# Kernel tuning notes

Hardware: AMD Instinct MI355X
Metric: run time of the kernel (lower is better)

Reference implementation:

```python
import jax, jax.numpy as jnp
import numpy as np

D = 2048
H = 16
HD = D // H
B = 2
T = 2048
EPS = 1e-6


def setup_inputs() -> dict:
    key = jax.random.key(0)
    ks = jax.random.split(key, 12)
    s = lambda fan_in: 1.0 / np.sqrt(fan_in)
    inp = {
        "x": jax.random.normal(ks[0], (B, T, D), dtype=jnp.float32),
        "mask": jnp.tril(jnp.ones((T, T), dtype=jnp.int32))[None, None],  # [1,1,T,T] causal
        "w_norm1": jnp.ones((D,), dtype=jnp.float32),
        "w_qkv": jax.random.normal(ks[1], (D, 3 * D), dtype=jnp.float32) * s(D),
        "b_qkv": jnp.zeros((3 * D,), dtype=jnp.float32),
        "w_proj": jax.random.normal(ks[2], (D, D), dtype=jnp.float32) * s(D),
        "b_proj": jnp.zeros((D,), dtype=jnp.float32),
        "w_norm2": jnp.ones((D,), dtype=jnp.float32),
        "w_fc1": jax.random.normal(ks[3], (D, 4 * D), dtype=jnp.float32) * s(D),
        "b_fc1": jnp.zeros((4 * D,), dtype=jnp.float32),
        "w_fc2": jax.random.normal(ks[4], (4 * D, D), dtype=jnp.float32) * s(4 * D),
        "b_fc2": jnpp_zeros((D,)) if False else jnp.zeros((D,), dtype=jnp.float32),
    }
    return inp


def _rmsnorm(x, w):
    # n = ||x||_2 / sqrt(d); out = x / (n + eps) * w  (matches source exactly)
    n = jnp.sqrt(jnp.sum(x * x, axis=-1, keepdims=True)) * (x.shape[-1] ** -0.5)
    return x / (n + EPS) * w


def _rope(q, k):
    # q,k: [B,H,T,HD]; half-split (non-interleaved) RoPE
    half = HD // 2
    idx = jnp.arange(half, dtype=jnp.float32)
    pos = jnp.arange(T, dtype=jnp.float32)[:, None]
    rates = jnp.power(10000.0, -2.0 * idx / HD)
    theta = pos * rates  # [T, half]
    cos, sin = jnp.cos(theta), jnp.sin(theta)

    def apply(x):
        x1, x2 = x[..., :half], x[..., half:]
        return jnp.concatenate([x1 * cos - x2 * sin, x1 * sin + x2 * cos], axis=-1)

    return apply(q), apply(k)


def reference(x, mask, w_norm1, w_qkv, b_qkv, w_proj, b_proj,
              w_norm2, w_fc1, b_fc1, w_fc2, b_fc2):
    # --- attention branch ---
    h = _rmsnorm(x, w_norm1)
    qkv = h @ w_qkv + b_qkv  # [B,T,3D]
    q, k, v = jnp.split(qkv, 3, axis=-1)
    q = q.reshape(B, T, H, HD).transpose(0, 2, 1, 3)
    k = k.reshape(B, T, H, HD).transpose(0, 2, 1, 3)
    v = v.reshape(B, T, H, HD).transpose(0, 2, 1, 3)
    q, k = _rope(q, k)
    att = jnp.einsum("bhqd,bhkd->bhqk", q, k) * (HD ** -0.5)
    att = jnp.where(mask == 0, -jnp.inf, att)
    att = jax.nn.softmax(att, axis=-1)
    y = jnp.einsum("bhqk,bhkd->bhqd", att, v)
    y = y.transpose(0, 2, 1, 3).reshape(B, T, D)
    x = x + (y @ w_proj + b_proj)
    # --- MLP branch ---
    h2 = _rmsnorm(x, w_norm2)
    h2 = jax.nn.silu(h2 @ w_fc1 + b_fc1)
    x = x + (h2 @ w_fc2 + b_fc2)
    return x
```

## Files before the change

### kernel.cpp

```cpp
#include <hip/hip_runtime.h>
#include <math.h>

typedef unsigned short u16;
typedef unsigned int u32;
typedef __attribute__((ext_vector_type(8))) short short8v;
typedef __attribute__((ext_vector_type(4))) float float4v;

#define T_SEQ 2048
#define D_MODEL 2048
#define N_HEADS 16
#define EPSV 1e-6f
#define MROWS 4096
#define MB (1024ull * 1024ull)

__device__ __forceinline__ u16 f2bf(float f) {
  union { float f; u32 u; } v; v.f = f;
  u32 r = v.u + 0x7fffu + ((v.u >> 16) & 1u);
  return (u16)(r >> 16);
}
__device__ __forceinline__ float bf2f(u16 h) {
  union { u32 u; float f; } v; v.u = ((u32)h) << 16;
  return v.f;
}
__device__ __forceinline__ void gl16(const void* g, void* l) {
  __builtin_amdgcn_global_load_lds(
      (const __attribute__((address_space(1))) void*)g,
      (__attribute__((address_space(3))) void*)l, 16, 0, 0);
}

__global__ __launch_bounds__(256) void rmsnorm_split_kernel(
    const float* __restrict__ x, const float* __restrict__ w,
    u16* __restrict__ oh, u16* __restrict__ ol) {
  const int row = blockIdx.x;
  const float* xr = x + (size_t)row * D_MODEL;

  float ss = 0.f;
#pragma unroll
  for (int it = 0; it < 2; ++it) {
    int i = threadIdx.x + it * 256;
    float4 v = ((const float4*)xr)[i];
    ss += v.x * v.x + v.y * v.y + v.z * v.z + v.w * v.w;
  }
#pragma unroll
  for (int off = 32; off >= 1; off >>= 1) ss += __shfl_xor(ss, off, 64);
  __shared__ float red[4];
  if ((threadIdx.x & 63) == 0) red[threadIdx.x >> 6] = ss;
  __syncthreads();
  const float tot = red[0] + red[1] + red[2] + red[3];
  const float n = sqrtf(tot) * 0.022097086912079608f;
  const float inv = 1.0f / (n + EPSV);

  u16* ohr = oh + (size_t)row * D_MODEL;
  u16* olr = ol + (size_t)row * D_MODEL;
#pragma unroll
  for (int it = 0; it < 2; ++it) {
    int i = threadIdx.x + it * 256;
    float4 v = ((const float4*)xr)[i];
    float4 wv = ((const float4*)w)[i];
    float o[4] = {v.x * inv * wv.x, v.y * inv * wv.y, v.z * inv * wv.z,
                  v.w * inv * wv.w};
    ushort4 h4, l4;
    h4.x = f2bf(o[0]); l4.x = f2bf(o[0] - bf2f(h4.x));
    h4.y = f2bf(o[1]); l4.y = f2bf(o[1] - bf2f(h4.y));
    h4.z = f2bf(o[2]); l4.z = f2bf(o[2] - bf2f(h4.z));
    h4.w = f2bf(o[3]); l4.w = f2bf(o[3] - bf2f(h4.w));
    ((ushort4*)ohr)[i] = h4;
    ((ushort4*)olr)[i] = l4;
  }
}

__global__ __launch_bounds__(256) void splitT_kernel(
    const float* __restrict__ W, u16* __restrict__ Th, u16* __restrict__ Tl,
    int K, int N) {
  __shared__ float tile[32][33];
  const int tx = threadIdx.x, ty = threadIdx.y;
  const int n0 = blockIdx.x * 32, k0 = blockIdx.y * 32;
#pragma unroll
  for (int i = 0; i < 4; ++i)
    tile[ty + i * 8][tx] = W[(size_t)(k0 + ty + i * 8) * N + n0 + tx];
  __syncthreads();
#pragma unroll
  for (int i = 0; i < 4; ++i) {
    const float v = tile[tx][ty + i * 8];
    const int n = n0 + ty + i * 8, k = k0 + tx;
    const u16 h = f2bf(v);
    Th[(size_t)n * K + k] = h;
    Tl[(size_t)n * K + k] = f2bf(v - bf2f(h));
  }
}

template <int OUT>
__global__ __launch_bounds__(256) void mgemm_kernel(
    const u16* __restrict__ Ah, const u16* __restrict__ Al,
    const u16* __restrict__ Bh, const u16* __restrict__ Bl,
    const float* __restrict__ bias, const float* __restrict__ res,
    float* __restrict__ C, u16* __restrict__ Ch, u16* __restrict__ Cl,
    int N, int K) {
  __shared__ __align__(16) u16 LAH[2][4096];
  __shared__ __align__(16) u16 LAL[2][4096];
  __shared__ __align__(16) u16 LBH[2][4096];
  __shared__ __align__(16) u16 LBL[2][4096];

  const int tid = threadIdx.x;
  const int lane = tid & 63;
  const int wv = tid >> 6;
  const int wr = wv >> 1, wc = wv & 1;

  const int gx = N >> 7;
  const int nwg = gx << 5;
  int id = blockIdx.x;
  id = (id & 7) * (nwg >> 3) + (id >> 3);
  const int g = id >> 7, w = id & 127;
  const int bn = (g << 2) + (w & 3);
  const int bm = w >> 2;

  const int srow = lane >> 2;
  const int scol = (lane & 3) << 3;
  const int c0 = wv * 2, c1 = c0 + 1;

  const size_t aoff0 = (size_t)(bm * 128 + c0 * 16 + srow) * K + scol;
  const size_t aoff1 = (size_t)(bm * 128 + c1 * 16 + srow) * K + scol;
  const size_t boff0 = (size_t)(bn * 128 + c0 * 16 + srow) * K + scol;
  const size_t boff1 = (size_t)(bn * 128 + c1 * 16 + srow) * K + scol;

  const int S = K >> 5;

  float4v acc[4][4];
  const float4v zf = {0.f, 0.f, 0.f, 0.f};
#pragma unroll
  for (int i = 0; i < 4; ++i)
#pragma unroll
    for (int j = 0; j < 4; ++j) acc[i][j] = zf;

  auto STAGE = [&](int buf, int step) {
    const size_t kk = (size_t)step << 5;
    gl16(Ah + aoff0 + kk, &LAH[buf][c0 << 9]);
    gl16(Ah + aoff1 + kk, &LAH[buf][c1 << 9]);
    gl16(Al + aoff0 + kk, &LAL[buf][c0 << 9]);
    gl16(Al + aoff1 + kk, &LAL[buf][c1 << 9]);
    gl16(Bh + boff0 + kk, &LBH[buf][c0 << 9]);
    gl16(Bh + boff1 + kk, &LBH[buf][c1 << 9]);
    gl16(Bl + boff0 + kk, &LBL[buf][c0 << 9]);
    gl16(Bl + boff1 + kk, &LBL[buf][c1 << 9]);
  };

  const int l15 = lane & 15;
  const int kq = lane >> 4;
  const int aoffc = (wr * 64 + l15) * 32 + kq * 8;
  const int boffc = (wc * 64 + l15) * 32 + kq * 8;

  auto COMPUTE = [&](int buf) {
    short8v bh[4], bl[4];
#pragma unroll
    for (int ni = 0; ni < 4; ++ni) {
      bh[ni] = *(const short8v*)&LBH[buf][boffc + ni * 512];
      bl[ni] = *(const short8v*)&LBL[buf][boffc + ni * 512];
    }
#pragma unroll
    for (int mi = 0; mi < 4; ++mi) {
      const short8v ah = *(const short8v*)&LAH[buf][aoffc + mi * 512];
      const short8v al = *(const short8v*)&LAL[buf][aoffc + mi * 512];
#pragma unroll
      for (int ni = 0; ni < 4; ++ni) {
        acc[mi][ni] = __builtin_amdgcn_mfma_f32_16x16x32_bf16(
            ah, bh[ni], acc[mi][ni], 0, 0, 0);
        acc[mi][ni] = __builtin_amdgcn_mfma_f32_16x16x32_bf16(
            al, bh[ni], acc[mi][ni], 0, 0, 0);
        acc[mi][ni] = __builtin_amdgcn_mfma_f32_16x16x32_bf16(
            ah, bl[ni], acc[mi][ni], 0, 0, 0);
      }
    }
  };

  STAGE(0, 0);
  __syncthreads();
  for (int step = 0; step < S - 1; ++step) {
    const int cur = step & 1;
    STAGE(cur ^ 1, step + 1);
    COMPUTE(cur);
    __syncthreads();
  }
  COMPUTE((S - 1) & 1);

  const int rsub = kq * 4;
#pragma unroll
  for (int mi = 0; mi < 4; ++mi) {
#pragma unroll
    for (int ni = 0; ni < 4; ++ni) {
      const int col = bn * 128 + wc * 64 + ni * 16 + l15;
      const float bb = bias[col];
      const float4v v = acc[mi][ni];
#pragma unroll
      for (int r = 0; r < 4; ++r) {
        const int row = bm * 128 + wr * 64 + mi * 16 + rsub + r;
        float val = v[r] + bb;
        if (OUT == 1) val += res[(size_t)row * N + col];
        if (OUT == 2) {
          const float sv = val / (1.f + expf(-val));
          const u16 hh = f2bf(sv);
          Ch[(size_t)row * N + col] = hh;
          Cl[(size_t)row * N + col] = f2bf(sv - bf2f(hh));
        } else {
          C[(size_t)row * N + col] = val;
        }
      }
    }
  }
}

__global__ __launch_bounds__(256) void rope_table_kernel(
    float* __restrict__ ct, float* __restrict__ st) {
  const int p = blockIdx.x * 256 + threadIdx.x;
  const int i = p & 63;
  const int t = p >> 6;
  const float ratef = (float)pow(10000.0, -(double)i / 64.0);
  const float theta = (float)t * ratef;
  ct[p] = (float)cos((double)theta);
  st[p] = (float)sin((double)theta);
}

__global__ __launch_bounds__(256) void rope_split_kernel(
    const float* __restrict__ qkv, const float* __restrict__ ct,
    const float* __restrict__ st, u16* __restrict__ Qh, u16* __restrict__ Ql,
    u16* __restrict__ Kh, u16* __restrict__ Kl, u16* __restrict__ Vth,
    u16* __restrict__ Vtl) {
  const int tt = blockIdx.x, bh = blockIdx.y;
  const int b = bh >> 4, h = bh & 15;
  const int tid = threadIdx.x;
  const int tl = tid >> 2, quad = tid & 3;
  const int t = tt * 64 + tl;
  const size_t rowbase = ((size_t)(b * T_SEQ + t)) * 6144 + h * 128;
  const size_t qkbase = (size_t)bh * T_SEQ * 128 + (size_t)t * 128;

#pragma unroll
  for (int i = 0; i < 4; ++i) {
    const int d0 = quad * 4 + i * 16;
    const float4 c4 = *(const float4*)&ct[(size_t)t * 64 + d0];
    const float4 s4 = *(const float4*)&st[(size_t)t * 64 + d0];
#pragma unroll
    for (int qk = 0; qk < 2; ++qk) {
      const size_t src = rowbase + qk * D_MODEL + d0;
      const float4 a = *(const float4*)&qkv[src];
      const float4 bb = *(const float4*)&qkv[src + 64];
      float o1[4] = {a.x * c4.x - bb.x * s4.x, a.y * c4.y - bb.y * s4.y,
                     a.z * c4.z - bb.z * s4.z, a.w * c4.w - bb.w * s4.w};
      float o2[4] = {a.x * s4.x + bb.x * c4.x, a.y * s4.y + bb.y * c4.y,
                     a.z * s4.z + bb.z * c4.z, a.w * s4.w + bb.w * c4.w};
      u16* dh = (qk == 0) ? Qh : Kh;
      u16* dl = (qk == 0) ? Ql : Kl;
      ushort4 h4, l4;
      h4.x = f2bf(o1[0]); l4.x = f2bf(o1[0] - bf2f(h4.x));
      h4.y = f2bf(o1[1]); l4.y = f2bf(o1[1] - bf2f(h4.y));
      h4.z = f2bf(o1[2]); l4.z = f2bf(o1[2] - bf2f(h4.z));
      h4.w = f2bf(o1[3]); l4.w = f2bf(o1[3] - bf2f(h4.w));
      *(ushort4*)&dh[qkbase + d0] = h4;
      *(ushort4*)&dl[qkbase + d0] = l4;
      h4.x = f2bf(o2[0]); l4.x = f2bf(o2[0] - bf2f(h4.x));
      h4.y = f2bf(o2[1]); l4.y = f2bf(o2[1] - bf2f(h4.y));
      h4.z = f2bf(o2[2]); l4.z = f2bf(o2[2] - bf2f(h4.z));
      h4.w = f2bf(o2[3]); l4.w = f2bf(o2[3] - bf2f(h4.w));
      *(ushort4*)&dh[qkbase + 64 + d0] = h4;
      *(ushort4*)&dl[qkbase + 64 + d0] = l4;
    }
  }

  __shared__ float Lv[64][132];
#pragma unroll
  for (int i = 0; i < 8; ++i) {
    const int c0 = quad * 4 + i * 16;
    const float4 v = *(const float4*)&qkv[rowbase + 2 * D_MODEL + c0];
    *(float4*)&Lv[tl][c0] = v;
  }
  __syncthreads();
  const int dd = tid >> 1, half = tid & 1;
  const size_t vtb =
      (size_t)bh * 128 * T_SEQ + (size_t)dd * T_SEQ + tt * 64 + half * 32;
#pragma unroll
  for (int g = 0; g < 4; ++g) {
    short8v hv, lv;
#pragma unroll
    for (int e = 0; e < 8; ++e) {
      const float v = Lv[half * 32 + g * 8 + e][dd];
      const u16 hh = f2bf(v);
      hv[e] = (short)hh;
      lv[e] = (short)f2bf(v - bf2f(hh));
    }
    *(short8v*)&Vth[vtb + g * 8] = hv;
    *(short8v*)&Vtl[vtb + g * 8] = lv;
  }
}

__global__ __launch_bounds__(256) void attn_mfma_kernel(
    const u16* __restrict__ Qh, const u16* __restrict__ Ql,
    const u16* __restrict__ Kh, const u16* __restrict__ Kl,
    const u16* __restrict__ Vth, const u16* __restrict__ Vtl,
    u16* __restrict__ yh, u16* __restrict__ yl) {
  __shared__ __align__(16) u16 lds[4][8192];
  int id = blockIdx.x;
  id = (id & 7) * 128 + (id >> 3);
  const int qt = id & 31, bh = id >> 5;
  const int tid = threadIdx.x, lane = tid & 63, wv = tid >> 6;
  const int l15 = lane & 15, kq = lane >> 4;

  const size_t hQK = (size_t)bh * T_SEQ * 128;
  const size_t hVt = (size_t)bh * 128 * T_SEQ;

  short8v qfh[4], qfl[4];
  {
    const size_t qb = hQK + (size_t)(qt * 64 + wv * 16 + l15) * 128 + kq * 8;
#pragma unroll
    for (int ks = 0; ks < 4; ++ks) {
      qfh[ks] = *(const short8v*)(Qh + qb + ks * 32);
      qfl[ks] = *(const short8v*)(Ql + qb + ks * 32);
    }
  }

  const float4v zf = {0.f, 0.f, 0.f, 0.f};
  float4v Oa[8];
#pragma unroll
  for (int i = 0; i < 8; ++i) Oa[i] = zf;
  float mM = -INFINITY, lS = 0.f;

  for (int kt = 0; kt <= qt; ++kt) {
    __syncthreads();
    if (wv < 2) {
      const u16* src = (wv == 0 ? Kh : Kl) + hQK + (size_t)kt * 64 * 128;
#pragma unroll
      for (int i = 0; i < 16; ++i) {
        const int off = i * 1024 + lane * 16;
        const int soff = off ^ (((off >> 8) & 7) << 4);
        gl16((const char*)src + soff, (char*)(&lds[wv][0]) + i * 1024);
      }
    } else {
      const u16* src = (wv == 2 ? Vth : Vtl) + hVt + (size_t)kt * 64;
#pragma unroll
      for (int i = 0; i < 16; ++i) {
        const int off = i * 1024 + lane * 16;
        const int d = off >> 7;
        const int soff = (off & 127) ^ ((d & 7) << 4);
        gl16((const char*)src + (size_t)d * 4096 + soff,
             (char*)(&lds[wv][0]) + i * 1024);
      }
    }
    __syncthreads();

    float4v sa[4];
#pragma unroll
    for (int i = 0; i < 4; ++i) sa[i] = zf;
#pragma unroll
    for (int ks = 0; ks < 4; ++ks) {
#pragma unroll
      for (int mf = 0; mf < 4; ++mf) {
        const int ro =
            ((mf * 16 + l15) * 256 + ks * 64 + kq * 16) ^ ((l15 & 7) << 4);
        const short8v kh = *(const short8v*)((const char*)(&lds[0][0]) + ro);
        const short8v kl = *(const short8v*)((const char*)(&lds[1][0]) + ro);
        sa[mf] = __builtin_amdgcn_mfma_f32_16x16x32_bf16(kh, qfh[ks], sa[mf], 0, 0, 0);
        sa[mf] = __builtin_amdgcn_mfma_f32_16x16x32_bf16(kl, qfh[ks], sa[mf], 0, 0, 0);
        sa[mf] = __builtin_amdgcn_mfma_f32_16x16x32_bf16(kh, qfl[ks], sa[mf], 0, 0, 0);
      }
    }

    const float scale = 0.08838834764831845f;
    const int qloc = wv * 16 + l15;
    float p[4][4];
    float pmax = -INFINITY;
#pragma unroll
    for (int mf = 0; mf < 4; ++mf)
#pragma unroll
      for (int r = 0; r < 4; ++r) {
        float v = sa[mf][r] * scale;
        if (kt == qt && (mf * 16 + kq * 4 + r) > qloc) v = -1e30f;
        p[mf][r] = v;
        pmax = fmaxf(pmax, v);
      }
    pmax = fmaxf(pmax, __shfl_xor(pmax, 16, 64));
    pmax = fmaxf(pmax, __shfl_xor(pmax, 32, 64));
    const float mnew = fmaxf(mM, pmax);
    const float alpha = __expf(mM - mnew);
    float rs = 0.f;
#pragma unroll
    for (int mf = 0; mf < 4; ++mf)
#pragma unroll
      for (int r = 0; r < 4; ++r) {
        const float pv = __expf(p[mf][r] - mnew);
        p[mf][r] = pv;
        rs += pv;
      }
    rs += __shfl_xor(rs, 16, 64);
    rs += __shfl_xor(rs, 32, 64);
    lS = lS * alpha + rs;
    mM = mnew;

    const int abase = (lane & 48) + ((lane >> 4) << 2);
    float al4[4];
#pragma unroll
    for (int r = 0; r < 4; ++r) al4[r] = __shfl(alpha, abase + r, 64);
#pragma unroll
    for (int nf = 0; nf < 8; ++nf)
#pragma unroll
      for (int r = 0; r < 4; ++r) Oa[nf][r] *= al4[r];

    short8v pah[2], pal[2];
#pragma unroll
    for (int ks2 = 0; ks2 < 2; ++ks2) {
#pragma unroll
      for (int j = 0; j < 8; ++j) {
        const int src = ((lane >> 4) & 1) * 32 + (j >> 2) * 16 + l15;
        const float va = __shfl(p[2 * ks2][j & 3], src, 64);
        const float vb = __shfl(p[2 * ks2 + 1][j & 3], src, 64);
        const float pj = (lane >= 32) ? vb : va;
        const u16 hh = f2bf(pj);
        pah[ks2][j] = (short)hh;
        pal[ks2][j] = (short)f2bf(pj - bf2f(hh));
      }
    }

#pragma unroll
    for (int nf = 0; nf < 8; ++nf) {
#pragma unroll
      for (int ks2 = 0; ks2 < 2; ++ks2) {
        const int ro =
            ((nf * 16 + l15) * 128 + ks2 * 64 + kq * 16) ^ ((l15 & 7) << 4);
        const short8v vh = *(const short8v*)((const char*)(&lds[2][0]) + ro);
        const short8v vl = *(const short8v*)((const char*)(&lds[3][0]) + ro);
        Oa[nf] = __builtin_amdgcn_mfma_f32_16x16x32_bf16(pah[ks2], vh, Oa[nf], 0, 0, 0);
        Oa[nf] = __builtin_amdgcn_mfma_f32_16x16x32_bf16(pal[ks2], vh, Oa[nf], 0, 0, 0);
        Oa[nf] = __builtin_amdgcn_mfma_f32_16x16x32_bf16(pah[ks2], vl, Oa[nf], 0, 0, 0);
      }
    }
  }

  const int abase = (lane & 48) + ((lane >> 4) << 2);
  float li[4];
#pragma unroll
  for (int r = 0; r < 4; ++r) li[r] = 1.f / __shfl(lS, abase + r, 64);
  const int b = bh >> 4, h = bh & 15;
#pragma unroll
  for (int r = 0; r < 4; ++r) {
    const int t = qt * 64 + wv * 16 + kq * 4 + r;
    const size_t ob = ((size_t)(b * T_SEQ + t)) * D_MODEL + h * 128 + l15;
#pragma unroll
    for (int nf = 0; nf < 8; ++nf) {
      const float val = Oa[nf][r] * li[r];
      const u16 hh = f2bf(val);
      yh[ob + nf * 16] = hh;
      yl[ob + nf * 16] = f2bf(val - bf2f(hh));
    }
  }
}

extern "C" void kernel_launch(void* const* d_in, const int* in_sizes, int n_in,
                              void* d_out, int out_size, void* d_ws,
                              size_t ws_size, hipStream_t stream) {
  const float* x       = (const float*)d_in[0];
  const float* w_norm1 = (const float*)d_in[2];
  const float* w_qkv   = (const float*)d_in[3];
  const float* b_qkv   = (const float*)d_in[4];
  const float* w_proj  = (const float*)d_in[5];
  const float* b_proj  = (const float*)d_in[6];
  const float* w_norm2 = (const float*)d_in[7];
  const float* w_fc1   = (const float*)d_in[8];
  const float* b_fc1   = (const float*)d_in[9];
  const float* w_fc2   = (const float*)d_in[10];
  const float* b_fc2   = (const float*)d_in[11];
  float* out = (float*)d_out;

  char* wsb = (char*)d_ws;
  float* qkvb = (float*)wsb;
  u16* fc1h = (u16*)wsb;
  u16* fc1l = (u16*)(wsb + 64 * MB);
  u16* qsh = (u16*)(wsb + 96 * MB);
  u16* qsl = (u16*)(wsb + 112 * MB);
  u16* ksh = (u16*)(wsb + 128 * MB);
  u16* ksl = (u16*)(wsb + 144 * MB);
  u16* vth = (u16*)(wsb + 160 * MB);
  u16* vtl = (u16*)(wsb + 176 * MB);
  u16* wth_qkv = (u16*)(wsb + 96 * MB);
  u16* wtl_qkv = (u16*)(wsb + 120 * MB);
  u16* wth_p = (u16*)(wsb + 96 * MB);
  u16* wtl_p = (u16*)(wsb + 104 * MB);
  u16* wth_f = (u16*)(wsb + 128 * MB);
  u16* wtl_f = (u16*)(wsb + 160 * MB);
  u16* ah = (u16*)(wsb + 192 * MB);
  u16* al = (u16*)(wsb + 208 * MB);
  u16* yh = ah;
  u16* yl = al;
  float* ct = (float*)(wsb + 224 * MB);
  float* st = ct + 131072;

  rope_table_kernel<<<512, 256, 0, stream>>>(ct, st);

  rmsnorm_split_kernel<<<4096, 256, 0, stream>>>(x, w_norm1, ah, al);
  splitT_kernel<<<dim3(192, 64), dim3(32, 8), 0, stream>>>(w_qkv, wth_qkv,
                                                           wtl_qkv, 2048, 6144);
  mgemm_kernel<0><<<dim3(48 * 32), 256, 0, stream>>>(
      ah, al, wth_qkv, wtl_qkv, b_qkv, nullptr, qkvb, nullptr, nullptr, 6144,
      2048);
  rope_split_kernel<<<dim3(32, 32), 256, 0, stream>>>(qkvb, ct, st, qsh, qsl,
                                                      ksh, ksl, vth, vtl);
  attn_mfma_kernel<<<dim3(1024), 256, 0, stream>>>(qsh, qsl, ksh, ksl, vth,
                                                   vtl, yh, yl);
  splitT_kernel<<<dim3(64, 64), dim3(32, 8), 0, stream>>>(w_proj, wth_p, wtl_p,
                                                          2048, 2048);
  mgemm_kernel<1><<<dim3(16 * 32), 256, 0, stream>>>(
      yh, yl, wth_p, wtl_p, b_proj, x, out, nullptr, nullptr, 2048, 2048);
  rmsnorm_split_kernel<<<4096, 256, 0, stream>>>(out, w_norm2, ah, al);
  splitT_kernel<<<dim3(256, 64), dim3(32, 8), 0, stream>>>(w_fc1, wth_f, wtl_f,
                                                           2048, 8192);
  mgemm_kernel<2><<<dim3(64 * 32), 256, 0, stream>>>(
      ah, al, wth_f, wtl_f, b_fc1, nullptr, nullptr, fc1h, fc1l, 8192, 2048);
  splitT_kernel<<<dim3(64, 256), dim3(32, 8), 0, stream>>>(w_fc2, wth_f, wtl_f,
                                                           8192, 2048);
  mgemm_kernel<1><<<dim3(16 * 32), 256, 0, stream>>>(
      fc1h, fc1l, wth_f, wtl_f, b_fc2, out, out, nullptr, nullptr, 2048, 8192);
}
```

Before: 1.836 ms.

## Enlarge split-bf16 GEMM tile to 256x128 with swizzled combined LDS and priority hints

The split-bf16 GEMM now runs 512 threads (8 waves) per block computing a 256x128 output tile, so each B tile is reused across twice as many rows. The high and low halves are interleaved into one XOR-swizzled LDS buffer to avoid bank conflicts. The K-loop replaces __syncthreads with an explicit vmcnt wait plus raw barriers, and wraps the MFMA burst in s_setprio. The intent is less global traffic per FLOP and better overlap of loads with MFMA work, at the cost of fewer workgroups per GEMM and a larger LDS footprint per block.

```diff
diff --git a/kernel.cpp b/kernel.cpp
--- a/kernel.cpp
+++ b/kernel.cpp
@@ -90,16 +90,13 @@
 }
 
 template <int OUT>
-__global__ __launch_bounds__(256) void mgemm_kernel(
+__global__ __launch_bounds__(512) void mgemm_kernel(
     const u16* __restrict__ Ah, const u16* __restrict__ Al,
     const u16* __restrict__ Bh, const u16* __restrict__ Bl,
     const float* __restrict__ bias, const float* __restrict__ res,
     float* __restrict__ C, u16* __restrict__ Ch, u16* __restrict__ Cl,
     int N, int K) {
-  __shared__ __align__(16) u16 LAH[2][4096];
-  __shared__ __align__(16) u16 LAL[2][4096];
-  __shared__ __align__(16) u16 LBH[2][4096];
-  __shared__ __align__(16) u16 LBL[2][4096];
+  __shared__ __align__(16) u16 lds[2][24576];
 
   const int tid = threadIdx.x;
   const int lane = tid & 63;
@@ -107,21 +104,28 @@
   const int wr = wv >> 1, wc = wv & 1;
 
   const int gx = N >> 7;
-  const int nwg = gx << 5;
+  const int nwg = gx << 4;
   int id = blockIdx.x;
   id = (id & 7) * (nwg >> 3) + (id >> 3);
-  const int g = id >> 7, w = id & 127;
+  const int g = id >> 6, w = id & 63;
   const int bn = (g << 2) + (w & 3);
   const int bm = w >> 2;
 
-  const int srow = lane >> 2;
-  const int scol = (lane & 3) << 3;
-  const int c0 = wv * 2, c1 = c0 + 1;
-
-  const size_t aoff0 = (size_t)(bm * 128 + c0 * 16 + srow) * K + scol;
-  const size_t aoff1 = (size_t)(bm * 128 + c1 * 16 + srow) * K + scol;
-  const size_t boff0 = (size_t)(bn * 128 + c0 * 16 + srow) * K + scol;
-  const size_t boff1 = (size_t)(bn * 128 + c1 * 16 + srow) * K + scol;
+  const int ls = lane >> 3;
+  const int ss = (lane & 7) ^ ls;
+  const int sel = ss >> 2;
+  const int sc = (ss & 3) << 3;
+
+  const u16* aS[4];
+  const u16* bS[2];
+#pragma unroll
+  for (int cc = 0; cc < 4; ++cc)
+    aS[cc] = (sel ? Al : Ah) +
+             (size_t)(bm * 256 + wv * 32 + cc * 8 + ls) * K + sc;
+#pragma unroll
+  for (int cc = 0; cc < 2; ++cc)
+    bS[cc] = (sel ? Bl : Bh) +
+             (size_t)(bn * 128 + wv * 16 + cc * 8 + ls) * K + sc;
 
   const int S = K >> 5;
 
@@ -133,54 +137,72 @@
     for (int j = 0; j < 4; ++j) acc[i][j] = zf;
 
   auto STAGE = [&](int buf, int step) {
-    const size_t kk = (size_t)step << 5;
-    gl16(Ah + aoff0 + kk, &LAH[buf][c0 << 9]);
-    gl16(Ah + aoff1 + kk, &LAH[buf][c1 << 9]);
-    gl16(Al + aoff0 + kk, &LAL[buf][c0 << 9]);
-    gl16(Al + aoff1 + kk, &LAL[buf][c1 << 9]);
-    gl16(Bh + boff0 + kk, &LBH[buf][c0 << 9]);
-    gl16(Bh + boff1 + kk, &LBH[buf][c1 << 9]);
-    gl16(Bl + boff0 + kk, &LBL[buf][c0 << 9]);
-    gl16(Bl + boff1 + kk, &LBL[buf][c1 << 9]);
+    const int kk = step << 5;
+    char* lb = (char*)&lds[buf][0];
+#pragma unroll
+    for (int cc = 0; cc < 4; ++cc)
+      gl16(aS[cc] + kk, lb + (wv * 4 + cc) * 1024);
+#pragma unroll
+    for (int cc = 0; cc < 2; ++cc)
+      gl16(bS[cc] + kk, lb + 32768 + (wv * 2 + cc) * 1024);
   };
 
   const int l15 = lane & 15;
   const int kq = lane >> 4;
-  const int aoffc = (wr * 64 + l15) * 32 + kq * 8;
-  const int boffc = (wc * 64 + l15) * 32 + kq * 8;
+  const int swz = (l15 & 7) << 4;
+  const int hOff = (kq * 16) ^ swz;
+  const int lOff = (64 + kq * 16) ^ swz;
+  int aRow[4], bRow[4];
+#pragma unroll
+  for (int mi = 0; mi < 4; ++mi) aRow[mi] = (wr * 64 + mi * 16 + l15) * 128;
+#pragma unroll
+  for (int ni = 0; ni < 4; ++ni)
+    bRow[ni] = 32768 + (wc * 64 + ni * 16 + l15) * 128;
 
   auto COMPUTE = [&](int buf) {
+    const char* lb = (const char*)&lds[buf][0];
     short8v bh[4], bl[4];
 #pragma unroll
     for (int ni = 0; ni < 4; ++ni) {
-      bh[ni] = *(const short8v*)&LBH[buf][boffc + ni * 512];
-      bl[ni] = *(const short8v*)&LBL[buf][boffc + ni * 512];
-    }
+      bh[ni] = *(const short8v*)(lb + bRow[ni] + hOff);
+      bl[ni] = *(const short8v*)(lb + bRow[ni] + lOff);
+    }
+    short8v ah[4], al[4];
 #pragma unroll
     for (int mi = 0; mi < 4; ++mi) {
-      const short8v ah = *(const short8v*)&LAH[buf][aoffc + mi * 512];
-      const short8v al = *(const short8v*)&LAL[buf][aoffc + mi * 512];
+      ah[mi] = *(const short8v*)(lb + aRow[mi] + hOff);
+      al[mi] = *(const short8v*)(lb + aRow[mi] + lOff);
+    }
+    __builtin_amdgcn_s_setprio(1);
+#pragma unroll
+    for (int mi = 0; mi < 4; ++mi) {
 #pragma unroll
       for (int ni = 0; ni < 4; ++ni) {
         acc[mi][ni] = __builtin_amdgcn_mfma_f32_16x16x32_bf16(
-            ah, bh[ni], acc[mi][ni], 0, 0, 0);
+            ah[mi], bh[ni], acc[mi][ni], 0, 0, 0);
         acc[mi][ni] = __builtin_amdgcn_mfma_f32_16x16x32_bf16(
-            al, bh[ni], acc[mi][ni], 0, 0, 0);
+            al[mi], bh[ni], acc[mi][ni], 0, 0, 0);
         acc[mi][ni] = __builtin_amdgcn_mfma_f32_16x16x32_bf16(
-            ah, bl[ni], acc[mi][ni], 0, 0, 0);
-      }
-    }
+            ah[mi], bl[ni], acc[mi][ni], 0, 0, 0);
+      }
+    }
+    __builtin_amdgcn_s_setprio(0);
   };
 
   STAGE(0, 0);
-  __syncthreads();
-  for (int step = 0; step < S - 1; ++step) {
-    const int cur = step & 1;
-    STAGE(cur ^ 1, step + 1);
-    COMPUTE(cur);
-    __syncthreads();
-  }
-  COMPUTE((S - 1) & 1);
+  int t = 0;
+  for (; t < S - 1; ++t) {
+    STAGE((t + 1) & 1, t + 1);
+    asm volatile("s_waitcnt vmcnt(6)" ::: "memory");
+    __builtin_amdgcn_s_barrier();
+    __builtin_amdgcn_sched_barrier(0);
+    COMPUTE(t & 1);
+    __builtin_amdgcn_s_barrier();
+  }
+  asm volatile("s_waitcnt vmcnt(0)" ::: "memory");
+  __builtin_amdgcn_s_barrier();
+  __builtin_amdgcn_sched_barrier(0);
+  COMPUTE(t & 1);
 
   const int rsub = kq * 4;
 #pragma unroll
@@ -192,7 +214,7 @@
       const float4v v = acc[mi][ni];
 #pragma unroll
       for (int r = 0; r < 4; ++r) {
-        const int row = bm * 128 + wr * 64 + mi * 16 + rsub + r;
+        const int row = bm * 256 + wr * 64 + mi * 16 + rsub + r;
         float val = v[r] + bb;
         if (OUT == 1) val += res[(size_t)row * N + col];
         if (OUT == 2) {
@@ -494,7 +516,7 @@
   rmsnorm_split_kernel<<<4096, 256, 0, stream>>>(x, w_norm1, ah, al);
   splitT_kernel<<<dim3(192, 64), dim3(32, 8), 0, stream>>>(w_qkv, wth_qkv,
                                                            wtl_qkv, 2048, 6144);
-  mgemm_kernel<0><<<dim3(48 * 32), 256, 0, stream>>>(
+  mgemm_kernel<0><<<dim3(48 * 16), 512, 0, stream>>>(
       ah, al, wth_qkv, wtl_qkv, b_qkv, nullptr, qkvb, nullptr, nullptr, 6144,
       2048);
   rope_split_kernel<<<dim3(32, 32), 256, 0, stream>>>(qkvb, ct, st, qsh, qsl,
@@ -503,15 +525,15 @@
                                                    vtl, yh, yl);
   splitT_kernel<<<dim3(64, 64), dim3(32, 8), 0, stream>>>(w_proj, wth_p, wtl_p,
                                                           2048, 2048);
-  mgemm_kernel<1><<<dim3(16 * 32), 256, 0, stream>>>(
+  mgemm_kernel<1><<<dim3(16 * 16), 512, 0, stream>>>(
       yh, yl, wth_p, wtl_p, b_proj, x, out, nullptr, nullptr, 2048, 2048);
   rmsnorm_split_kernel<<<4096, 256, 0, stream>>>(out, w_norm2, ah, al);
   splitT_kernel<<<dim3(256, 64), dim3(32, 8), 0, stream>>>(w_fc1, wth_f, wtl_f,
                                                            2048, 8192);
-  mgemm_kernel<2><<<dim3(64 * 32), 256, 0, stream>>>(
+  mgemm_kernel<2><<<dim3(64 * 16), 512, 0, stream>>>(
       ah, al, wth_f, wtl_f, b_fc1, nullptr, nullptr, fc1h, fc1l, 8192, 2048);
   splitT_kernel<<<dim3(64, 256), dim3(32, 8), 0, stream>>>(w_fc2, wth_f, wtl_f,
                                                            8192, 2048);
-  mgemm_kernel<1><<<dim3(16 * 32), 256, 0, stream>>>(
+  mgemm_kernel<1><<<dim3(16 * 16), 512, 0, stream>>>(
       fc1h, fc1l, wth_f, wtl_f, b_fc2, out, out, nullptr, nullptr, 2048, 8192);
 }
```

New measurement: 1.669 ms. 9.1% less time.
